# Kernel optimization log

Hardware: AMD Instinct MI355X
Metric: run time of the kernel (lower is better)

## Reference

```python
import jax, jax.numpy as jnp
import numpy as np

K = 32  # neighbors per point (self.k)

def setup_inputs() -> dict:
    key = jax.random.key(0)
    k1, k2 = jax.random.split(key)
    B, N, C = 16, 4096, 64
    x = jax.random.normal(k1, (B, N, C), dtype=jnp.float32)
    idx = jax.random.randint(k2, (B, N, K), 0, N, dtype=jnp.int64)
    return {"x": x, "idx": idx}

def reference(x, idx):
    # pooled[b, n, :] = mean_k x[b, idx[b, n, k], :]
    # gather per-batch: xb[ib] -> [N, K, C]
    gathered = jax.vmap(lambda xb, ib: xb[ib])(x, idx)  # [B, N, K, C]
    return gathered.mean(axis=2)  # [B, N, C]
```

## Files before the change

### kernel.cpp

```cpp
#include <hip/hip_runtime.h>


#define BB 16
#define NN 4096
#define KK 32
#define CC 64
#define CH8 8
#define NCHUNK (CC / CH8)
#define NQ 4
#define PTS (NN / NQ)
#define THREADS 512
#define IDX16_ELEMS (BB * NN * KK)
#define PREP_BLOCKS 2048
#define PREP_THREADS 256

#define GLOBAL_AS __attribute__((address_space(1)))
#define LDS_AS    __attribute__((address_space(3)))

__device__ __forceinline__ uint pk_bf16(float a, float b) {
    uint ua = __float_as_uint(a);
    ua = (ua + 0x7fffu + ((ua >> 16) & 1u)) >> 16;
    uint ub = __float_as_uint(b);
    ub = (ub + 0x7fffu + ((ub >> 16) & 1u)) & 0xffff0000u;
    return ua | ub;
}

__global__ __launch_bounds__(PREP_THREADS)
void prep_kernel(const float* __restrict__ x,
                 const int* __restrict__ idx32,
                 ushort* __restrict__ idx16,
                 uint4* __restrict__ xbf) {
    int vprobe = idx32[2 * (threadIdx.x & 63) + 1];
    const int is64 = (__ballot(vprobe != 0) == 0ULL) ? 1 : 0;

    const int tid = blockIdx.x * blockDim.x + threadIdx.x;
    const int stride = gridDim.x * blockDim.x;

    if (is64) {
        const int4* __restrict__ in = (const int4*)idx32;
        uint* __restrict__ o = (uint*)idx16;
        for (int i = tid; i < IDX16_ELEMS / 2; i += stride) {
            int4 v = in[i];
            o[i] = (uint)(v.x & 0xFFFF) | ((uint)(v.z & 0xFFFF) << 16);
        }
    } else {
        const int4* __restrict__ in = (const int4*)idx32;
        uint2* __restrict__ o = (uint2*)idx16;
        for (int i = tid; i < IDX16_ELEMS / 4; i += stride) {
            int4 v = in[i];
            o[i] = make_uint2((uint)(v.x & 0xFFFF) | ((uint)(v.y & 0xFFFF) << 16),
                              (uint)(v.z & 0xFFFF) | ((uint)(v.w & 0xFFFF) << 16));
        }
    }

    {
        const int u = tid;
        const int row = u >> 3;
        const int ch = u & 7;
        const int b = row >> 12;
        const int n = row & (NN - 1);
        const float4* __restrict__ x4 = (const float4*)x;
        const float4 v0 = x4[(size_t)row * (CC / 4) + ch * 2];
        const float4 v1 = x4[(size_t)row * (CC / 4) + ch * 2 + 1];
        xbf[(size_t)(b * NCHUNK + ch) * NN + n] =
            make_uint4(pk_bf16(v0.x, v0.y), pk_bf16(v0.z, v0.w),
                       pk_bf16(v1.x, v1.y), pk_bf16(v1.z, v1.w));
    }
}

__device__ __forceinline__ void acc8(float a[8], uint4 r) {
    a[0] += __uint_as_float(r.x << 16);
    a[1] += __uint_as_float(r.x & 0xffff0000u);
    a[2] += __uint_as_float(r.y << 16);
    a[3] += __uint_as_float(r.y & 0xffff0000u);
    a[4] += __uint_as_float(r.z << 16);
    a[5] += __uint_as_float(r.z & 0xffff0000u);
    a[6] += __uint_as_float(r.w << 16);
    a[7] += __uint_as_float(r.w & 0xffff0000u);
}

__global__ __launch_bounds__(THREADS, 4)
void gapool_bf16_kernel(const ushort* __restrict__ idx16,
                        const uint4* __restrict__ xbf,
                        float* __restrict__ out) {
    __shared__ uint4 tile[NN];

    const int bid = blockIdx.x;
    const int b = bid & 15;
    const int g = bid >> 4;
    const int chunk = g & (NCHUNK - 1);
    const int q = g >> 3;
    const int tid = threadIdx.x;
    const float s = 1.0f / KK;

    const ushort* __restrict__ idxq =
        idx16 + ((size_t)b * NN + (size_t)q * PTS) * KK;
    float* __restrict__ outq =
        out + ((size_t)b * NN + (size_t)q * PTS) * CC + chunk * CH8;
    const uint4* __restrict__ src = xbf + (size_t)(b * NCHUNK + chunk) * NN;

    const uint4* __restrict__ ip0 = (const uint4*)(idxq + (size_t)tid * KK);
    uint4 pa = ip0[0], pb = ip0[1], pc = ip0[2], pd = ip0[3];

    {
        const GLOBAL_AS uint* gsrc = (const GLOBAL_AS uint*)src;
        LDS_AS uint* ltile = (LDS_AS uint*)tile;
#pragma unroll
        for (int i = 0; i < NN / THREADS; ++i) {
            const int r = i * THREADS + tid;
            __builtin_amdgcn_global_load_lds(gsrc + (size_t)r * 4,
                                             ltile + (size_t)r * 4, 16, 0, 0);
        }
    }
    __syncthreads();

    for (int p = tid; p < PTS; p += THREADS) {
        const uint w[16] = {pa.x, pa.y, pa.z, pa.w, pb.x, pb.y, pb.z, pb.w,
                            pc.x, pc.y, pc.z, pc.w, pd.x, pd.y, pd.z, pd.w};
        if (p + THREADS < PTS) {
            const uint4* ipn =
                (const uint4*)(idxq + (size_t)(p + THREADS) * KK);
            pa = ipn[0]; pb = ipn[1]; pc = ipn[2]; pd = ipn[3];
        }

        float a[8] = {0.f, 0.f, 0.f, 0.f, 0.f, 0.f, 0.f, 0.f};
#pragma unroll
        for (int i = 0; i < 16; ++i) {
            acc8(a, tile[w[i] & 0xFFFFu]);
            acc8(a, tile[w[i] >> 16]);
        }

        float4* op = (float4*)(outq + (size_t)p * CC);
        op[0] = make_float4(a[0] * s, a[1] * s, a[2] * s, a[3] * s);
        op[1] = make_float4(a[4] * s, a[5] * s, a[6] * s, a[7] * s);
    }
}

extern "C" void kernel_launch(void* const* d_in, const int* in_sizes, int n_in,
                              void* d_out, int out_size, void* d_ws, size_t ws_size,
                              hipStream_t stream) {
    const float* x     = (const float*)d_in[0];
    const int*   idx32 = (const int*)d_in[1];
    float*       out   = (float*)d_out;
    ushort*      idx16 = (ushort*)d_ws;
    uint4*       xbf   = (uint4*)((char*)d_ws + IDX16_ELEMS * 2);

    prep_kernel<<<PREP_BLOCKS, PREP_THREADS, 0, stream>>>(x, idx32, idx16, xbf);

    gapool_bf16_kernel<<<BB * NCHUNK * NQ, THREADS, 0, stream>>>(
        idx16, xbf, out);
}
```

Measured before the change: 87.45 us.

## Split each point across four lanes reading 4-byte LDS words

Each point's 8-channel bf16 chunk is now processed by four threads, each reading one 32-bit word per neighbor from LDS instead of one thread reading a 16-byte uint4. This is meant to reduce LDS bank conflicts from random 16-byte gathers and to cut per-thread register pressure. The cost is that each thread reloads the same 32 indices, and every loop iteration issues four times as many index loads and narrower float2 stores.

After: 88.95 us. No clear change (+1.7%).

```diff
diff --git a/kernel.cpp b/kernel.cpp
--- a/kernel.cpp
+++ b/kernel.cpp
@@ -10,6 +10,7 @@
 #define NQ 4
 #define PTS (NN / NQ)
 #define THREADS 512
+#define NSLOT (THREADS / 4)
 #define IDX16_ELEMS (BB * NN * KK)
 #define PREP_BLOCKS 2048
 #define PREP_THREADS 256
@@ -68,22 +69,11 @@
     }
 }
 
-__device__ __forceinline__ void acc8(float a[8], uint4 r) {
-    a[0] += __uint_as_float(r.x << 16);
-    a[1] += __uint_as_float(r.x & 0xffff0000u);
-    a[2] += __uint_as_float(r.y << 16);
-    a[3] += __uint_as_float(r.y & 0xffff0000u);
-    a[4] += __uint_as_float(r.z << 16);
-    a[5] += __uint_as_float(r.z & 0xffff0000u);
-    a[6] += __uint_as_float(r.w << 16);
-    a[7] += __uint_as_float(r.w & 0xffff0000u);
-}
-
 __global__ __launch_bounds__(THREADS, 4)
 void gapool_bf16_kernel(const ushort* __restrict__ idx16,
                         const uint4* __restrict__ xbf,
                         float* __restrict__ out) {
-    __shared__ uint4 tile[NN];
+    __shared__ uint tile[NN * 4];
 
     const int bid = blockIdx.x;
     const int b = bid & 15;
@@ -91,15 +81,17 @@
     const int chunk = g & (NCHUNK - 1);
     const int q = g >> 3;
     const int tid = threadIdx.x;
+    const int c2 = tid & 3;
+    const int slot = tid >> 2;
     const float s = 1.0f / KK;
 
     const ushort* __restrict__ idxq =
         idx16 + ((size_t)b * NN + (size_t)q * PTS) * KK;
     float* __restrict__ outq =
-        out + ((size_t)b * NN + (size_t)q * PTS) * CC + chunk * CH8;
+        out + ((size_t)b * NN + (size_t)q * PTS) * CC + chunk * CH8 + c2 * 2;
     const uint4* __restrict__ src = xbf + (size_t)(b * NCHUNK + chunk) * NN;
 
-    const uint4* __restrict__ ip0 = (const uint4*)(idxq + (size_t)tid * KK);
+    const uint4* __restrict__ ip0 = (const uint4*)(idxq + (size_t)slot * KK);
     uint4 pa = ip0[0], pb = ip0[1], pc = ip0[2], pd = ip0[3];
 
     {
@@ -114,25 +106,32 @@
     }
     __syncthreads();
 
-    for (int p = tid; p < PTS; p += THREADS) {
+#pragma unroll
+    for (int j = 0; j < PTS / NSLOT; ++j) {
+        const int p = j * NSLOT + slot;
         const uint w[16] = {pa.x, pa.y, pa.z, pa.w, pb.x, pb.y, pb.z, pb.w,
                             pc.x, pc.y, pc.z, pc.w, pd.x, pd.y, pd.z, pd.w};
-        if (p + THREADS < PTS) {
+        if (j + 1 < PTS / NSLOT) {
             const uint4* ipn =
-                (const uint4*)(idxq + (size_t)(p + THREADS) * KK);
+                (const uint4*)(idxq + (size_t)(p + NSLOT) * KK);
             pa = ipn[0]; pb = ipn[1]; pc = ipn[2]; pd = ipn[3];
         }
 
-        float a[8] = {0.f, 0.f, 0.f, 0.f, 0.f, 0.f, 0.f, 0.f};
+        float a0 = 0.f, a1 = 0.f;
 #pragma unroll
         for (int i = 0; i < 16; ++i) {
-            acc8(a, tile[w[i] & 0xFFFFu]);
-            acc8(a, tile[w[i] >> 16]);
+            const uint lo = w[i] & 0xFFFFu;
+            const uint hi = w[i] >> 16;
+            const uint d0 = tile[lo * 4 + c2];
+            const uint d1 = tile[hi * 4 + c2];
+            a0 += __uint_as_float(d0 << 16);
+            a1 += __uint_as_float(d0 & 0xffff0000u);
+            a0 += __uint_as_float(d1 << 16);
+            a1 += __uint_as_float(d1 & 0xffff0000u);
         }
 
-        float4* op = (float4*)(outq + (size_t)p * CC);
-        op[0] = make_float4(a[0] * s, a[1] * s, a[2] * s, a[3] * s);
-        op[1] = make_float4(a[4] * s, a[5] * s, a[6] * s, a[7] * s);
+        float2* op = (float2*)(outq + (size_t)p * CC);
+        *op = make_float2(a0 * s, a1 * s);
     }
 }
 
```

## Fuse prep into gather kernel, reading raw fp32 x and raw indices directly

Applied to the files above, without the earlier changes.

Drops the separate prep kernel that compressed the indices to 16 bits and converted x to a bf16 chunked layout. The main kernel now loads fp32 x rows, converts them to bf16 into LDS itself, and reads the original int32/int64 indices directly, with the 32- vs 64-bit width chosen by a ballot probe. This removes one launch and the write and re-read of the intermediate buffers. In exchange each block reads 2x wider x data with a strided access pattern, and the 64-bit case reads 4x more index bytes, without the register prefetch of the next point's indices.

After: 91.33 us. +4.4%, slower.

```diff
diff --git a/kernel.cpp b/kernel.cpp
--- a/kernel.cpp
+++ b/kernel.cpp
@@ -10,12 +10,6 @@
 #define NQ 4
 #define PTS (NN / NQ)
 #define THREADS 512
-#define IDX16_ELEMS (BB * NN * KK)
-#define PREP_BLOCKS 2048
-#define PREP_THREADS 256
-
-#define GLOBAL_AS __attribute__((address_space(1)))
-#define LDS_AS    __attribute__((address_space(3)))
 
 __device__ __forceinline__ uint pk_bf16(float a, float b) {
     uint ua = __float_as_uint(a);
@@ -23,49 +17,6 @@
     uint ub = __float_as_uint(b);
     ub = (ub + 0x7fffu + ((ub >> 16) & 1u)) & 0xffff0000u;
     return ua | ub;
-}
-
-__global__ __launch_bounds__(PREP_THREADS)
-void prep_kernel(const float* __restrict__ x,
-                 const int* __restrict__ idx32,
-                 ushort* __restrict__ idx16,
-                 uint4* __restrict__ xbf) {
-    int vprobe = idx32[2 * (threadIdx.x & 63) + 1];
-    const int is64 = (__ballot(vprobe != 0) == 0ULL) ? 1 : 0;
-
-    const int tid = blockIdx.x * blockDim.x + threadIdx.x;
-    const int stride = gridDim.x * blockDim.x;
-
-    if (is64) {
-        const int4* __restrict__ in = (const int4*)idx32;
-        uint* __restrict__ o = (uint*)idx16;
-        for (int i = tid; i < IDX16_ELEMS / 2; i += stride) {
-            int4 v = in[i];
-            o[i] = (uint)(v.x & 0xFFFF) | ((uint)(v.z & 0xFFFF) << 16);
-        }
-    } else {
-        const int4* __restrict__ in = (const int4*)idx32;
-        uint2* __restrict__ o = (uint2*)idx16;
-        for (int i = tid; i < IDX16_ELEMS / 4; i += stride) {
-            int4 v = in[i];
-            o[i] = make_uint2((uint)(v.x & 0xFFFF) | ((uint)(v.y & 0xFFFF) << 16),
-                              (uint)(v.z & 0xFFFF) | ((uint)(v.w & 0xFFFF) << 16));
-        }
-    }
-
-    {
-        const int u = tid;
-        const int row = u >> 3;
-        const int ch = u & 7;
-        const int b = row >> 12;
-        const int n = row & (NN - 1);
-        const float4* __restrict__ x4 = (const float4*)x;
-        const float4 v0 = x4[(size_t)row * (CC / 4) + ch * 2];
-        const float4 v1 = x4[(size_t)row * (CC / 4) + ch * 2 + 1];
-        xbf[(size_t)(b * NCHUNK + ch) * NN + n] =
-            make_uint4(pk_bf16(v0.x, v0.y), pk_bf16(v0.z, v0.w),
-                       pk_bf16(v1.x, v1.y), pk_bf16(v1.z, v1.w));
-    }
 }
 
 __device__ __forceinline__ void acc8(float a[8], uint4 r) {
@@ -80,9 +31,9 @@
 }
 
 __global__ __launch_bounds__(THREADS, 4)
-void gapool_bf16_kernel(const ushort* __restrict__ idx16,
-                        const uint4* __restrict__ xbf,
-                        float* __restrict__ out) {
+void gapool_fused(const float* __restrict__ x,
+                  const int* __restrict__ idx32,
+                  float* __restrict__ out) {
     __shared__ uint4 tile[NN];
 
     const int bid = blockIdx.x;
@@ -93,46 +44,62 @@
     const int tid = threadIdx.x;
     const float s = 1.0f / KK;
 
-    const ushort* __restrict__ idxq =
-        idx16 + ((size_t)b * NN + (size_t)q * PTS) * KK;
-    float* __restrict__ outq =
-        out + ((size_t)b * NN + (size_t)q * PTS) * CC + chunk * CH8;
-    const uint4* __restrict__ src = xbf + (size_t)(b * NCHUNK + chunk) * NN;
-
-    const uint4* __restrict__ ip0 = (const uint4*)(idxq + (size_t)tid * KK);
-    uint4 pa = ip0[0], pb = ip0[1], pc = ip0[2], pd = ip0[3];
+    int vprobe = idx32[2 * (tid & 63) + 1];
+    const bool is64 = (__ballot(vprobe != 0) == 0ULL);
 
     {
-        const GLOBAL_AS uint* gsrc = (const GLOBAL_AS uint*)src;
-        LDS_AS uint* ltile = (LDS_AS uint*)tile;
+        const float4* __restrict__ x4 =
+            (const float4*)x + (size_t)b * NN * (CC / 4) + chunk * 2;
 #pragma unroll
         for (int i = 0; i < NN / THREADS; ++i) {
             const int r = i * THREADS + tid;
-            __builtin_amdgcn_global_load_lds(gsrc + (size_t)r * 4,
-                                             ltile + (size_t)r * 4, 16, 0, 0);
+            const float4 v0 = x4[(size_t)r * (CC / 4)];
+            const float4 v1 = x4[(size_t)r * (CC / 4) + 1];
+            tile[r] = make_uint4(pk_bf16(v0.x, v0.y), pk_bf16(v0.z, v0.w),
+                                 pk_bf16(v1.x, v1.y), pk_bf16(v1.z, v1.w));
         }
     }
     __syncthreads();
 
-    for (int p = tid; p < PTS; p += THREADS) {
-        const uint w[16] = {pa.x, pa.y, pa.z, pa.w, pb.x, pb.y, pb.z, pb.w,
-                            pc.x, pc.y, pc.z, pc.w, pd.x, pd.y, pd.z, pd.w};
-        if (p + THREADS < PTS) {
-            const uint4* ipn =
-                (const uint4*)(idxq + (size_t)(p + THREADS) * KK);
-            pa = ipn[0]; pb = ipn[1]; pc = ipn[2]; pd = ipn[3];
+    const size_t pbase = (size_t)b * NN + (size_t)q * PTS;
+    float* __restrict__ outq = out + pbase * CC + chunk * CH8;
+
+    if (is64) {
+        const uint4* __restrict__ ib = (const uint4*)idx32 + pbase * (KK / 2);
+#pragma unroll
+        for (int pp = 0; pp < PTS / THREADS; ++pp) {
+            const int p = pp * THREADS + tid;
+            const uint4* __restrict__ ip = ib + (size_t)p * (KK / 2);
+            float a[8] = {0.f, 0.f, 0.f, 0.f, 0.f, 0.f, 0.f, 0.f};
+#pragma unroll
+            for (int t = 0; t < KK / 2; ++t) {
+                const uint4 w = ip[t];
+                acc8(a, tile[w.x]);
+                acc8(a, tile[w.z]);
+            }
+            float4* op = (float4*)(outq + (size_t)p * CC);
+            op[0] = make_float4(a[0] * s, a[1] * s, a[2] * s, a[3] * s);
+            op[1] = make_float4(a[4] * s, a[5] * s, a[6] * s, a[7] * s);
         }
-
-        float a[8] = {0.f, 0.f, 0.f, 0.f, 0.f, 0.f, 0.f, 0.f};
+    } else {
+        const uint4* __restrict__ ib = (const uint4*)idx32 + pbase * (KK / 4);
 #pragma unroll
-        for (int i = 0; i < 16; ++i) {
-            acc8(a, tile[w[i] & 0xFFFFu]);
-            acc8(a, tile[w[i] >> 16]);
+        for (int pp = 0; pp < PTS / THREADS; ++pp) {
+            const int p = pp * THREADS + tid;
+            const uint4* __restrict__ ip = ib + (size_t)p * (KK / 4);
+            float a[8] = {0.f, 0.f, 0.f, 0.f, 0.f, 0.f, 0.f, 0.f};
+#pragma unroll
+            for (int t = 0; t < KK / 4; ++t) {
+                const uint4 w = ip[t];
+                acc8(a, tile[w.x]);
+                acc8(a, tile[w.y]);
+                acc8(a, tile[w.z]);
+                acc8(a, tile[w.w]);
+            }
+            float4* op = (float4*)(outq + (size_t)p * CC);
+            op[0] = make_float4(a[0] * s, a[1] * s, a[2] * s, a[3] * s);
+            op[1] = make_float4(a[4] * s, a[5] * s, a[6] * s, a[7] * s);
         }
-
-        float4* op = (float4*)(outq + (size_t)p * CC);
-        op[0] = make_float4(a[0] * s, a[1] * s, a[2] * s, a[3] * s);
-        op[1] = make_float4(a[4] * s, a[5] * s, a[6] * s, a[7] * s);
     }
 }
 
@@ -142,11 +109,7 @@
     const float* x     = (const float*)d_in[0];
     const int*   idx32 = (const int*)d_in[1];
     float*       out   = (float*)d_out;
-    ushort*      idx16 = (ushort*)d_ws;
-    uint4*       xbf   = (uint4*)((char*)d_ws + IDX16_ELEMS * 2);
+    (void)d_ws; (void)ws_size;
 
-    prep_kernel<<<PREP_BLOCKS, PREP_THREADS, 0, stream>>>(x, idx32, idx16, xbf);
-
-    gapool_bf16_kernel<<<BB * NCHUNK * NQ, THREADS, 0, stream>>>(
-        idx16, xbf, out);
+    gapool_fused<<<BB * NCHUNK * NQ, THREADS, 0, stream>>>(x, idx32, out);
 }
```
